# Optimization experiments

Hardware: AMD Instinct MI355X
Metric: run time of the kernel (lower is better)

Reference implementation:

```python
import jax, jax.numpy as jnp
import numpy as np

B, N, K = 2, 1024, 16
D_MODEL, D_ELLIP, N_HEADS = 768, 128, 8
NF = D_MODEL // 6            # sinusoidal freqs per coordinate
MAX_LOG_FREQ = 7.0
ENC_H = max(1, N_HEADS // 2) # ellipsoid encoder heads
ENC_FF = 2048                # torch TransformerEncoderLayer default dim_feedforward


def setup_inputs() -> dict:
    key = jax.random.key(0)
    ks = jax.random.split(key, 20)
    rn = lambda k, sh, sc=1.0: jax.random.normal(k, sh, dtype=jnp.float32) * sc
    w = lambda k, o, i: rn(k, (o, i), 1.0 / np.sqrt(i))
    inp = {}
    inp['s'] = rn(ks[0], (B, N, D_MODEL))
    inp['R'] = rn(ks[1], (B, N, 3, 3))
    inp['t'] = rn(ks[2], (B, N, 3))
    inp['ellip_tokens'] = rn(ks[3], (B, K, D_ELLIP))
    inp['mu'] = rn(ks[4], (B, K, 3))
    inp['Sigma'] = rn(ks[5], (B, K, 3, 3))
    inp['ellip_mask'] = jnp.ones((B, K), dtype=jnp.bool_)
    # main attention params (torch Linear convention: [out, in])
    inp['mix_w'] = w(ks[6], 6 * NF, 6 * NF)
    inp['lin_cov_w'] = w(ks[7], D_MODEL, 9)
    inp['q_w'] = w(ks[8], D_MODEL, D_MODEL)
    inp['k_w'] = w(ks[9], D_MODEL, 2 * D_MODEL)
    inp['v_w'] = w(ks[10], D_MODEL, D_MODEL + D_ELLIP)
    inp['o_w'] = w(ks[11], D_MODEL, D_MODEL)
    # ellipsoid TransformerEncoderLayer params (post-norm, eval mode)
    inp['enc_in_w'] = w(ks[12], 3 * D_ELLIP, D_ELLIP)
    inp['enc_in_b'] = jnp.zeros((3 * D_ELLIP,), jnp.float32)
    inp['enc_out_w'] = w(ks[13], D_ELLIP, D_ELLIP)
    inp['enc_out_b'] = jnp.zeros((D_ELLIP,), jnp.float32)
    inp['lin1_w'] = w(ks[14], ENC_FF, D_ELLIP)
    inp['lin1_b'] = jnp.zeros((ENC_FF,), jnp.float32)
    inp['lin2_w'] = w(ks[15], D_ELLIP, ENC_FF)
    inp['lin2_b'] = jnp.zeros((D_ELLIP,), jnp.float32)
    inp['ln1_g'] = jnp.ones((D_ELLIP,), jnp.float32)
    inp['ln1_b'] = jnp.zeros((D_ELLIP,), jnp.float32)
    inp['ln2_g'] = jnp.ones((D_ELLIP,), jnp.float32)
    inp['ln2_b'] = jnp.zeros((D_ELLIP,), jnp.float32)
    return inp


def _layernorm(x, g, b, eps=1e-5):
    m = x.mean(-1, keepdims=True)
    v = ((x - m) ** 2).mean(-1, keepdims=True)
    return (x - m) / jnp.sqrt(v + eps) * g + b


def _fwd(s, R, t, ellip_tokens, mu, Sigma, mix_w, lin_cov_w, q_w, k_w, v_w, o_w,
         enc_in_w, enc_in_b, enc_out_w, enc_out_b, lin1_w, lin1_b, lin2_w, lin2_b,
         ln1_g, ln1_b, ln2_g, ln2_b, ellip_mask):
    # --- ellipsoid self-attn encoder (single post-norm layer, eval mode) ---
    x = ellip_tokens                                   # [B,K,de]
    qkv = x @ enc_in_w.T + enc_in_b
    q, kk, v = jnp.split(qkv, 3, axis=-1)
    dhe = D_ELLIP // ENC_H
    qh = q.reshape(B, K, ENC_H, dhe)
    kh = kk.reshape(B, K, ENC_H, dhe)
    vh = v.reshape(B, K, ENC_H, dhe)
    sc = jnp.einsum('bqhd,bkhd->bhqk', qh, kh) / np.sqrt(dhe).astype(np.float32)
    ao = jnp.einsum('bhqk,bkhd->bqhd', jax.nn.softmax(sc, -1), vh).reshape(B, K, D_ELLIP)
    ao = ao @ enc_out_w.T + enc_out_b
    x = _layernorm(x + ao, ln1_g, ln1_b)
    ff = jax.nn.relu(x @ lin1_w.T + lin1_b) @ lin2_w.T + lin2_b
    e = _layernorm(x + ff, ln2_g, ln2_b)               # [B,K,de]
    # --- per-query local frame transforms ---
    diff = mu[:, None, :, :] - t[:, :, None, :]        # [B,N,K,3]
    r = jnp.einsum('bnji,bnkj->bnki', R, diff)         # R^T @ diff
    C = jnp.einsum('bnji,bkjl,bnlm->bnkim', R, Sigma, R)  # R^T Sigma R [B,N,K,3,3]
    # --- sinusoidal posenc (sin first, then cos; flatten coord-major) ---
    freqs = 2.0 ** jnp.linspace(0.0, MAX_LOG_FREQ, NF).astype(jnp.float32)
    xf = r[..., None] * freqs                          # [B,N,K,3,NF]
    feat = jnp.concatenate([jnp.sin(xf), jnp.cos(xf)], axis=-2).reshape(B, N, K, 6 * NF)
    pos = feat @ mix_w.T                               # [B,N,K,d]
    cov = C.reshape(B, N, K, 9) @ lin_cov_w.T          # [B,N,K,d]
    K_mat = jnp.concatenate([pos, cov], -1) @ k_w.T    # [B,N,K,d]
    eB = jnp.broadcast_to(e[:, None, :, :], (B, N, K, D_ELLIP))
    V_mat = jnp.concatenate([pos, eB], -1) @ v_w.T     # [B,N,K,d]
    Q = s @ q_w.T                                      # [B,N,d]
    dh = D_MODEL // N_HEADS
    Qh = Q.reshape(B, N, N_HEADS, dh)
    Kh = K_mat.reshape(B, N, K, N_HEADS, dh)
    Vh = V_mat.reshape(B, N, K, N_HEADS, dh)
    scores = jnp.einsum('bnhd,bnkhd->bnhk', Qh, Kh) / np.sqrt(dh).astype(np.float32)
    scores = scores + (1.0 - ellip_mask.astype(scores.dtype))[:, None, None, :] * -10000.0
    attn = jax.nn.softmax(scores, -1)                  # [B,N,H,K]
    out = jnp.einsum('bnhk,bnkhd->bnhd', attn, Vh).reshape(B, N, D_MODEL)
    return out @ o_w.T


def reference(s, R, t, ellip_tokens, mu, Sigma, mix_w, lin_cov_w, q_w, k_w, v_w, o_w,
              enc_in_w, enc_in_b, enc_out_w, enc_out_b, lin1_w, lin1_b, lin2_w, lin2_b,
              ln1_g, ln1_b, ln2_g, ln2_b, ellip_mask):
    return _fwd(s, R, t, ellip_tokens, mu, Sigma, mix_w, lin_cov_w, q_w, k_w, v_w, o_w,
                enc_in_w, enc_in_b, enc_out_w, enc_out_b, lin1_w, lin1_b, lin2_w, lin2_b,
                ln1_g, ln1_b, ln2_g, ln2_b, ellip_mask)
```

## Files before the change

### kernel.cpp

```cpp
#include <hip/hip_runtime.h>
#include <math.h>

#define BB     2
#define SEQ    1024
#define KTOK   16
#define DM     768
#define DE     128
#define NH     8
#define DHD    96
#define EH     4
#define DHE    32
#define EFF    2048

typedef short short8 __attribute__((ext_vector_type(8)));
typedef float f32x4 __attribute__((ext_vector_type(4)));
typedef unsigned short ushort_t;

__device__ __forceinline__ void split2(float x, ushort_t& h, ushort_t& l) {
  unsigned u = __float_as_uint(x);
  unsigned hb = (u + 0x7fffu + ((u >> 16) & 1u)) >> 16;
  float hf = __uint_as_float(hb << 16);
  float r = x - hf;
  unsigned u2 = __float_as_uint(r);
  unsigned lb = (u2 + 0x7fffu + ((u2 >> 16) & 1u)) >> 16;
  h = (ushort_t)hb;
  l = (ushort_t)lb;
}

typedef const unsigned int __attribute__((address_space(1)))* gas_p;
typedef unsigned int __attribute__((address_space(3)))* las_p;
__device__ __forceinline__ void load_lds16(const ushort_t* g, ushort_t* l) {
  __builtin_amdgcn_global_load_lds((gas_p)g, (las_p)l, 16, 0, 0);
}

template<int OMODE, bool ADD>
__device__ __forceinline__ void gemm_body(
    ushort_t (*AhB)[2048], ushort_t (*AlB)[2048],
    ushort_t (*BhB)[2048], ushort_t (*BlB)[2048],
    const ushort_t* A, int lda, int aC0, int aLoOff,
    const ushort_t* B, int ldb, int bC0, int bLoOff,
    void* Cv, int ldc, int cLoOff,
    const float* av, int ldadd,
    int row0, int col0, int N, int K)
{
  int tid = threadIdx.x;
  int wave = tid >> 6, lane = tid & 63;
  int quad = lane >> 4, mrow = lane & 15;
  int wm = (wave >> 1) * 32, wn = (wave & 1) * 32;
  int sr = tid >> 2, q8 = (tid & 3) << 3;
  int wbase = wave << 9;
  f32x4 acc[2][2] = {};

  const ushort_t* pa = A + (long)(row0 + sr) * lda + (aC0 + q8);
  const ushort_t* pb = B + (long)(col0 + sr) * ldb + (bC0 + q8);

  load_lds16(pa, &AhB[0][wbase]);
  load_lds16(pa + aLoOff, &AlB[0][wbase]);
  load_lds16(pb, &BhB[0][wbase]);
  load_lds16(pb + bLoOff, &BlB[0][wbase]);

  int buf = 0;
  for (int k0 = 0; k0 < K; k0 += 32) {
    __syncthreads();
    if (k0 + 32 < K) {
      int kn = k0 + 32;
      load_lds16(pa + kn, &AhB[buf ^ 1][wbase]);
      load_lds16(pa + aLoOff + kn, &AlB[buf ^ 1][wbase]);
      load_lds16(pb + kn, &BhB[buf ^ 1][wbase]);
      load_lds16(pb + bLoOff + kn, &BlB[buf ^ 1][wbase]);
    }
    short8 fah[2], fal[2], fbh[2], fbl[2];
    #pragma unroll
    for (int t = 0; t < 2; t++) {
      fah[t] = *(const short8*)&AhB[buf][(wm + t * 16 + mrow) * 32 + (quad << 3)];
      fal[t] = *(const short8*)&AlB[buf][(wm + t * 16 + mrow) * 32 + (quad << 3)];
      fbh[t] = *(const short8*)&BhB[buf][(wn + t * 16 + mrow) * 32 + (quad << 3)];
      fbl[t] = *(const short8*)&BlB[buf][(wn + t * 16 + mrow) * 32 + (quad << 3)];
    }
    #pragma unroll
    for (int mt = 0; mt < 2; mt++)
      #pragma unroll
      for (int nt = 0; nt < 2; nt++) {
        f32x4 c = acc[mt][nt];
        c = __builtin_amdgcn_mfma_f32_16x16x32_bf16(fah[mt], fbh[nt], c, 0, 0, 0);
        c = __builtin_amdgcn_mfma_f32_16x16x32_bf16(fal[mt], fbh[nt], c, 0, 0, 0);
        c = __builtin_amdgcn_mfma_f32_16x16x32_bf16(fah[mt], fbl[nt], c, 0, 0, 0);
        acc[mt][nt] = c;
      }
    buf ^= 1;
  }
  float* Cf = (float*)Cv;
  ushort_t* Cs = (ushort_t*)Cv;
  #pragma unroll
  for (int mt = 0; mt < 2; mt++)
    #pragma unroll
    for (int nt = 0; nt < 2; nt++) {
      int col = col0 + wn + nt * 16 + mrow;
      if (col >= N) continue;
      int rb = row0 + wm + mt * 16 + (quad << 2);
      #pragma unroll
      for (int rr = 0; rr < 4; rr++) {
        float v = acc[mt][nt][rr];
        if (ADD) v += av[(long)(rb + rr) * ldadd + col];
        if (OMODE == 0) {
          Cf[(long)(rb + rr) * ldc + col] = v;
        } else {
          ushort_t h, l;
          split2(v, h, l);
          Cs[(long)(rb + rr) * ldc + col] = h;
          Cs[(long)(rb + rr) * ldc + cLoOff + col] = l;
        }
      }
    }
}

template<int OMODE, bool ADD>
__global__ __launch_bounds__(256) void gemm3t(
    const ushort_t* __restrict__ A, int lda, int aKstep, int aLoOff,
    const ushort_t* __restrict__ B, long bOffZ, int ldb, int bKstep, int bLoOff,
    void* __restrict__ Cv, int ldc, int cOffZ, int cLoOff,
    const float* __restrict__ addv, int ldadd, int addOffZ,
    int M, int N, int K)
{
  __shared__ ushort_t Ah[2][2048], Al[2][2048], Bh[2][2048], Bl[2][2048];
  int z = blockIdx.z;
  void* Cz = (OMODE == 0) ? (void*)((float*)Cv + (long)z * cOffZ)
                          : (void*)((ushort_t*)Cv + (long)z * cOffZ);
  gemm_body<OMODE, ADD>(Ah, Al, Bh, Bl,
      A, lda, z * aKstep, aLoOff,
      B + (long)z * bOffZ, ldb, z * bKstep, bLoOff,
      Cz, ldc, cLoOff,
      ADD ? addv + (long)z * addOffZ : nullptr, ldadd,
      blockIdx.y * 64, blockIdx.x * 64, N, K);
}

__global__ __launch_bounds__(256) void combo1(
    const float* __restrict__ s, const float* __restrict__ q_w,
    const float* __restrict__ o_w, const float* __restrict__ k_w,
    const float* __restrict__ v_w,
    ushort_t* __restrict__ sS, ushort_t* __restrict__ qwS,
    ushort_t* __restrict__ owS, ushort_t* __restrict__ kwS,
    ushort_t* __restrict__ vwS,
    const float* __restrict__ mix_w, ushort_t* __restrict__ mixTS,
    const float* __restrict__ tok, const float* __restrict__ enc_in_w,
    const float* __restrict__ enc_in_b, float* __restrict__ qkv,
    const float* __restrict__ lin_cov_w, float* __restrict__ Bk9)
{
  int r = blockIdx.x, tid = threadIdx.x;
// ... 61 lines not shown
      int rr = idx / 9, p = idx % 9;
      const float* kr = k_w + (long)rr * (2 * DM) + DM;
      float acc = 0.f;
      for (int j = 0; j < DM; j++) acc = fmaf(kr[j], lin_cov_w[j * 9 + p], acc);
      Bk9[idx] = acc;
    }
  }
}

__global__ __launch_bounds__(256) void mega1(
    const ushort_t* __restrict__ sS, const ushort_t* __restrict__ qwS,
    const ushort_t* __restrict__ mixTS, const ushort_t* __restrict__ kwS,
    const ushort_t* __restrict__ vwS,
    ushort_t* __restrict__ QS, ushort_t* __restrict__ AkTS,
    ushort_t* __restrict__ AvS,
    const float* __restrict__ t2e, const float* __restrict__ ln2_g,
    const float* __restrict__ ln2_b, const float* __restrict__ v_w,
    float* __restrict__ evec)
{
  __shared__ ushort_t Ah[2][2048], Al[2][2048], Bh[2][2048], Bl[2][2048];
  int r = blockIdx.x, tid = threadIdx.x;
  if (r < 384) {
    gemm_body<1, false>(Ah, Al, Bh, Bl, sS, 1536, 0, DM, qwS, 1536, 0, DM,
                        QS, 1536, DM, nullptr, 0, (r / 12) * 64, (r % 12) * 64, DM, DM);
  } else if (r < 528) {
    int t2 = r - 384;
    gemm_body<1, false>(Ah, Al, Bh, Bl, mixTS, 1536, 0, DM, kwS, 1536, 0, DM,
                        AkTS, 1536, DM, nullptr, 0, (t2 / 12) * 64, (t2 % 12) * 64, DM, DM);
  } else if (r < 672) {
    int t2 = r - 528;
    gemm_body<1, false>(Ah, Al, Bh, Bl, vwS, 1536, 0, DM, mixTS, 1536, 0, DM,
                        AvS, 1536, DM, nullptr, 0, (t2 / 12) * 64, (t2 % 12) * 64, DM, DM);
  } else {
    __shared__ float el[DE];
    __shared__ float red[4];
    __shared__ float stats[2];
    int idx = r - 672;
    float val = (tid < DE) ? t2e[idx * DE + tid] : 0.f;
    {
      float v = val;
      #pragma unroll
      for (int off = 32; off > 0; off >>= 1) v += __shfl_down(v, off);
      if ((tid & 63) == 0) red[tid >> 6] = v;
      __syncthreads();
      if (tid == 0) stats[0] = (red[0] + red[1] + red[2] + red[3]) * (1.f / DE);
      __syncthreads();
      float d = (tid < DE) ? (val - stats[0]) : 0.f;
      float v2 = d * d;
      #pragma unroll
      for (int off = 32; off > 0; off >>= 1) v2 += __shfl_down(v2, off);
      if ((tid & 63) == 0) red[tid >> 6] = v2;
      __syncthreads();
      if (tid == 0) stats[1] = rsqrtf((red[0] + red[1] + red[2] + red[3]) * (1.f / DE) + 1e-5f);
      __syncthreads();
      if (tid < DE) el[tid] = (val - stats[0]) * stats[1] * ln2_g[tid] + ln2_b[tid];
      __syncthreads();
    }
    #pragma unroll
    for (int q = 0; q < 3; q++) {
      int d = tid + (q << 8);
      float acc = 0.f;
      const float4* wr = (const float4*)(v_w + (long)d * (DM + DE) + DM);
      #pragma unroll 8
      for (int j = 0; j < DE / 4; j++) {
        float4 p = wr[j];
        acc = fmaf(p.x, el[j * 4 + 0], acc);
        acc = fmaf(p.y, el[j * 4 + 1], acc);
        acc = fmaf(p.z, el[j * 4 + 2], acc);
        acc = fmaf(p.w, el[j * 4 + 3], acc);
      }
      evec[idx * DM + d] = acc;
    }
  }
}

__global__ __launch_bounds__(256) void qa_qb(
    const ushort_t* __restrict__ QS, const ushort_t* __restrict__ AkTS,
    float* __restrict__ QA, const float* __restrict__ Bk9,
    float* __restrict__ QB)
{
  __shared__ ushort_t Ah[2][2048], Al[2][2048], Bh[2][2048], Bl[2][2048];
  int r = blockIdx.x;
  if (r < 3072) {
    int z = r / 384, rr = r % 384;
    gemm_body<0, false>(Ah, Al, Bh, Bl,
        QS, 1536, z * DHD, DM, AkTS, 1536, z * DHD, DM,
        (void*)(QA + (long)z * DM), NH * DM, 0, nullptr, 0,
        (rr / 12) * 64, (rr % 12) * 64, DM, DHD);
  } else {
    int idx = (r - 3072) * 256 + threadIdx.x;
    if (idx < BB * SEQ * NH * 9) {
      int bn = idx / 72, rem = idx % 72, h = rem / 9, p = rem % 9;
      const ushort_t* qr = QS + (long)bn * 1536 + h * DHD;
      float acc = 0.f;
      for (int k = 0; k < DHD; k++) {
        float q = __uint_as_float((unsigned)qr[k] << 16) +
                  __uint_as_float((unsigned)qr[DM + k] << 16);
        acc = fmaf(q, Bk9[(h * DHD + k) * 9 + p], acc);
      }
      QB[idx] = acc;
    }
  }
}

__global__ __launch_bounds__(128) void enc_attn_ln1(
    const float* __restrict__ tok, const float* __restrict__ qkvG,
    const float* __restrict__ out_w, const float* __restrict__ out_b,
    const float* __restrict__ ln1_g, const float* __restrict__ ln1_b,
    float* __restrict__ x1G)
{
  int idx = blockIdx.x;
  int b = idx >> 4, tk = idx & 15;
  int tid = threadIdx.x;
  __shared__ float qkvs[KTOK][384];
  __shared__ float ao[DE];
  __shared__ float scl[EH][KTOK], attnl[EH][KTOK];
  __shared__ float red[2];
  __shared__ float stats[2];
  for (int i = tid; i < KTOK * 384; i += 128)
    qkvs[i / 384][i % 384] = qkvG[b * KTOK * 384 + i];
  __syncthreads();
  if (tid < EH * KTOK) {
    int h = tid >> 4, kk = tid & 15;
    float acc = 0.f;
    #pragma unroll 8
    for (int d = 0; d < DHE; d++)
      acc = fmaf(qkvs[tk][h * DHE + d], qkvs[kk][DE + h * DHE + d], acc);
    scl[h][kk] = acc * 0.17677669529663687f;
  }
  __syncthreads();
  if (tid < EH) {
    float m = -1e30f;
    for (int kk = 0; kk < KTOK; kk++) m = fmaxf(m, scl[tid][kk]);
    float s = 0.f;
    for (int kk = 0; kk < KTOK; kk++) { float e = expf(scl[tid][kk] - m); attnl[tid][kk] = e; s += e; }
    float inv = 1.f / s;
    for (int kk = 0; kk < KTOK; kk++) attnl[tid][kk] *= inv;
  }
  __syncthreads();
  {
    int h = tid / DHE;
    float acc = 0.f;
    #pragma unroll
    for (int kk = 0; kk < KTOK; kk++) acc = fmaf(attnl[h][kk], qkvs[kk][256 + tid], acc);
    ao[tid] = acc;
  }
  __syncthreads();
  float val;
  {
    float acc = out_b[tid];
    const float4* wr = (const float4*)(out_w + (long)tid * DE);
    #pragma unroll 8
    for (int j = 0; j < DE / 4; j++) {
      float4 p = wr[j];
      acc = fmaf(p.x, ao[j * 4 + 0], acc);
      acc = fmaf(p.y, ao[j * 4 + 1], acc);
      acc = fmaf(p.z, ao[j * 4 + 2], acc);
      acc = fmaf(p.w, ao[j * 4 + 3], acc);
    }
    val = tok[idx * DE + tid] + acc;
  }
  {
    float v = val;
    #pragma unroll
    for (int off = 32; off > 0; off >>= 1) v += __shfl_down(v, off);
    if ((tid & 63) == 0) red[tid >> 6] = v;
    __syncthreads();
    if (tid == 0) stats[0] = (red[0] + red[1]) * (1.f / DE);
    __syncthreads();
    float d = val - stats[0];
    float v2 = d * d;
    #pragma unroll
    for (int off = 32; off > 0; off >>= 1) v2 += __shfl_down(v2, off);
    if ((tid & 63) == 0) red[tid >> 6] = v2;
    __syncthreads();
    if (tid == 0) stats[1] = rsqrtf((red[0] + red[1]) * (1.f / DE) + 1e-5f);
    __syncthreads();
    x1G[idx * DE + tid] = (val - stats[0]) * stats[1] * ln1_g[tid] + ln1_b[tid];
  }
}

__global__ __launch_bounds__(256) void enc_ff1(
    const float* __restrict__ x1G, const float* __restrict__ lin1_w,
    const float* __restrict__ lin1_b, float* __restrict__ ff1G)
{
  int tkn = blockIdx.x >> 3;
  int f = ((blockIdx.x & 7) << 8) + threadIdx.x;
  __shared__ float xs[DE];
  if (threadIdx.x < DE) xs[threadIdx.x] = x1G[tkn * DE + threadIdx.x];
  __syncthreads();
  float acc = lin1_b[f];
  const float4* wr = (const float4*)(lin1_w + (long)f * DE);
  #pragma unroll 8
  for (int j = 0; j < DE / 4; j++) {
    float4 p = wr[j];
    acc = fmaf(p.x, xs[j * 4 + 0], acc);
    acc = fmaf(p.y, xs[j * 4 + 1], acc);
    acc = fmaf(p.z, xs[j * 4 + 2], acc);
    acc = fmaf(p.w, xs[j * 4 + 3], acc);
  }
  ff1G[tkn * EFF + f] = fmaxf(acc, 0.f);
}

__global__ __launch_bounds__(256) void enc_ff2(
    const float* __restrict__ x1G, const float* __restrict__ ff1G,
    const float* __restrict__ lin2_w, const float* __restrict__ lin2_b,
    float* __restrict__ tmp2G)
{
  int wv = (blockIdx.x << 2) + (threadIdx.x >> 6);
  int tkn = wv >> 7, j = wv & 127;
  int lane = threadIdx.x & 63;
  const float* wr = lin2_w + (long)j * EFF;
  const float* fr = ff1G + (long)tkn * EFF;
  float acc = 0.f;
  #pragma unroll 8
  for (int i = 0; i < EFF / 64; i++) {
    int p = (i << 6) + lane;
    acc = fmaf(wr[p], fr[p], acc);
  }
  #pragma unroll
  for (int off = 32; off > 0; off >>= 1) acc += __shfl_down(acc, off);
  if (lane == 0)
    tmp2G[tkn * DE + j] = x1G[tkn * DE + j] + lin2_b[j] + acc;
}

__global__ __launch_bounds__(256) void main_attn(
    const float* __restrict__ Rg, const float* __restrict__ tg,
    const float* __restrict__ mug, const float* __restrict__ Sigg,
    const float* __restrict__ QAg, const float* __restrict__ QBg,
    const float* __restrict__ evec, ushort_t* __restrict__ wfeatS,
    float* __restrict__ outeG)
{
  int bn = blockIdx.x;
  int b = bn >> 10;
  int tid = threadIdx.x;
  int w = tid >> 6, lane = tid & 63;
  int h0 = 2 * w, h1 = 2 * w + 1;
  __shared__ float Rm[9], tm[3];
  __shared__ float rK[KTOK][3];
  __shared__ float C9[KTOK][9];
  __shared__ float featL[8][772];
  __shared__ float QBl[NH][12];
  __shared__ float scl[NH][KTOK];
  __shared__ float attnl[NH][KTOK];
  __shared__ float freqsL[128];
  float qa0[12], qa1[12];
  {
    const float* qbase = QAg + (long)bn * (NH * DM);
    #pragma unroll
    for (int i = 0; i < 12; i++) {
      qa0[i] = qbase[h0 * DM + i * 64 + lane];
      qa1[i] = qbase[h1 * DM + i * 64 + lane];
    }
  }
  if (tid < 9) Rm[tid] = Rg[bn * 9 + tid];
  if (tid >= 16 && tid < 19) tm[tid - 16] = tg[bn * 3 + (tid - 16)];
  if (tid >= 32 && tid < 32 + NH * 9) {
    int q = tid - 32;
    QBl[q / 9][q % 9] = QBg[bn * (NH * 9) + q];
  }
  if (tid >= 128) {
    const float step = 7.0f / 127.0f;
    freqsL[tid - 128] = exp2f(step * (float)(tid - 128));
  }
  __syncthreads();
  if (tid < KTOK) {
    int k = tid;
// ... 18 lines not shown
        for (int l = 0; l < 3; l++) a = fmaf(Sg[j * 3 + l], Rm[l * 3 + m2], a);
        SR[j * 3 + m2] = a;
      }
    #pragma unroll
    for (int i = 0; i < 3; i++)
      #pragma unroll
      for (int m2 = 0; m2 < 3; m2++) {
        float a = 0.f;
        #pragma unroll
        for (int j = 0; j < 3; j++) a = fmaf(Rm[j * 3 + i], SR[j * 3 + m2], a);
        C9[k][i * 3 + m2] = a;
      }
  }
  __syncthreads();
  for (int half = 0; half < 2; half++) {
    for (int i = tid; i < 8 * 384; i += 256) {
      int k = i / 384, jj = i % 384;
      int coord = jj >> 7, f = jj & 127;
      float xf = rK[half * 8 + k][coord] * freqsL[f];
      float sv, cv;
      __sincosf(xf, &sv, &cv);
      featL[k][jj] = sv;
      featL[k][jj + 384] = cv;
    }
    __syncthreads();
    for (int k = 0; k < 8; k++) {
      float a0 = 0.f, a1 = 0.f;
      #pragma unroll
      for (int i = 0; i < 12; i++) {
        float fv = featL[k][i * 64 + lane];
        a0 = fmaf(qa0[i], fv, a0);
        a1 = fmaf(qa1[i], fv, a1);
      }
      #pragma unroll
      for (int off = 32; off > 0; off >>= 1) {
        a0 += __shfl_down(a0, off);
        a1 += __shfl_down(a1, off);
      }
      if (lane == 0) { scl[h0][half * 8 + k] = a0; scl[h1][half * 8 + k] = a1; }
    }
    __syncthreads();
  }
  if (tid < NH) {
    int h = tid;
    float vals[KTOK];
    float m = -1e30f;
    for (int k = 0; k < KTOK; k++) {
      float a = scl[h][k];
      #pragma unroll
      for (int p = 0; p < 9; p++) a = fmaf(C9[k][p], QBl[h][p], a);
      a *= 0.10206207261596575f;
      vals[k] = a;
      m = fmaxf(m, a);
    }
    float s = 0.f;
    for (int k = 0; k < KTOK; k++) { float e = expf(vals[k] - m); attnl[h][k] = e; s += e; }
    float inv = 1.f / s;
    for (int k = 0; k < KTOK; k++) attnl[h][k] *= inv;
  }
  __syncthreads();
  float wf0[12], wf1[12];
  #pragma unroll
  for (int i = 0; i < 12; i++) { wf0[i] = 0.f; wf1[i] = 0.f; }
  for (int pass = 0; pass < 2; pass++) {
    int kb = (pass == 0) ? 8 : 0;
    if (pass == 1) {
      __syncthreads();
      for (int i = tid; i < 8 * 384; i += 256) {
        int k = i / 384, jj = i % 384;
        int coord = jj >> 7, f = jj & 127;
        float xf = rK[k][coord] * freqsL[f];
        float sv, cv;
        __sincosf(xf, &sv, &cv);
        featL[k][jj] = sv;
        featL[k][jj + 384] = cv;
      }
      __syncthreads();
    }
    #pragma unroll
    for (int i = 0; i < 12; i++) {
      int jj = i * 64 + lane;
      float s0 = wf0[i], s1 = wf1[i];
      #pragma unroll
      for (int k = 0; k < 8; k++) {
        float fv = featL[k][jj];
        s0 = fmaf(attnl[h0][kb + k], fv, s0);
        s1 = fmaf(attnl[h1][kb + k], fv, s1);
      }
      wf0[i] = s0; wf1[i] = s1;
    }
  }
  {
    ushort_t* wrow = wfeatS + (long)bn * (2 * NH * DM);
    #pragma unroll
    for (int i = 0; i < 12; i++) {
      int jj = i * 64 + lane;
      ushort_t h, l;
      split2(wf0[i], h, l);
      wrow[h0 * DM + jj] = h;
      wrow[NH * DM + h0 * DM + jj] = l;
      split2(wf1[i], h, l);
      wrow[h1 * DM + jj] = h;
      wrow[NH * DM + h1 * DM + jj] = l;
    }
  }
  for (int d = tid; d < DM; d += 256) {
    int h = d / DHD;
    float acc = 0.f;
    #pragma unroll
    for (int k = 0; k < KTOK; k++)
      acc = fmaf(attnl[h][k], evec[(b * KTOK + k) * DM + d], acc);
    outeG[(long)bn * DM + d] = acc;
  }
}

extern "C" void kernel_launch(void* const* d_in, const int* in_sizes, int n_in,
                              void* d_out, int out_size, void* d_ws, size_t ws_size,
                              hipStream_t stream) {
// ... 14 lines not shown
  const float* enc_out_w = (const float*)d_in[15];
  const float* enc_out_b = (const float*)d_in[16];
  const float* lin1_w = (const float*)d_in[17];
  const float* lin1_b = (const float*)d_in[18];
  const float* lin2_w = (const float*)d_in[19];
  const float* lin2_b = (const float*)d_in[20];
  const float* ln1_g = (const float*)d_in[21];
  const float* ln1_b = (const float*)d_in[22];
  const float* ln2_g = (const float*)d_in[23];
  const float* ln2_b = (const float*)d_in[24];
  float* out = (float*)d_out;
  char* wsb  = (char*)d_ws;

  const int BN = BB * SEQ;
  float* qkv  = (float*)(wsb);
  float* x1e  = (float*)(wsb + 49152);
  float* ff1e = (float*)(wsb + 65536);
  float* t2e  = (float*)(wsb + 327680);
  float* evec = (float*)(wsb + 344064);
  float* Bk9  = (float*)(wsb + 442368);
  char* p = wsb + 470016;
  ushort_t* qwS   = (ushort_t*)p;  p += 2359296;
  ushort_t* owS   = (ushort_t*)p;  p += 2359296;
  ushort_t* kwS   = (ushort_t*)p;  p += 2359296;
  ushort_t* vwS   = (ushort_t*)p;  p += 2359296;
  ushort_t* mixTS = (ushort_t*)p;  p += 2359296;
  ushort_t* AkTS  = (ushort_t*)p;  p += 2359296;
  ushort_t* AvS   = (ushort_t*)p;  p += 2359296;
  ushort_t* sS    = (ushort_t*)p;  p += 6291456;
  ushort_t* QS    = (ushort_t*)p;  p += 6291456;
  float*    QB    = (float*)p;     p += 589824;
  float*    oute  = (float*)p;     p += 6291456;
  float*    QA    = (float*)p;     p += 50331648;
  ushort_t* wfeatS = (ushort_t*)QA;
  ushort_t* US     = sS;

  dim3 blk(256);

  combo1<<<4043, blk, 0, stream>>>(s, q_w, o_w, k_w, v_w,
                                   sS, qwS, owS, kwS, vwS,
                                   mix_w, mixTS,
                                   tok, enc_in_w, enc_in_b, qkv,
                                   lin_cov_w, Bk9);
  enc_attn_ln1<<<BB * KTOK, dim3(128), 0, stream>>>(tok, qkv, enc_out_w, enc_out_b,
                                                    ln1_g, ln1_b, x1e);
  enc_ff1<<<256, blk, 0, stream>>>(x1e, lin1_w, lin1_b, ff1e);
  enc_ff2<<<1024, blk, 0, stream>>>(x1e, ff1e, lin2_w, lin2_b, t2e);
  mega1<<<704, blk, 0, stream>>>(sS, qwS, mixTS, kwS, vwS,
                                 QS, AkTS, AvS,
                                 t2e, ln2_g, ln2_b, v_w, evec);
  qa_qb<<<3648, blk, 0, stream>>>(QS, AkTS, QA, Bk9, QB);
  main_attn<<<BN, blk, 0, stream>>>(R, t, mu, Sig, QA, QB, evec, wfeatS, oute);
  gemm3t<1, true><<<dim3(2, 32, NH), blk, 0, stream>>>(
      wfeatS, 2 * NH * DM, DM, NH * DM,  AvS, (long)DHD * 1536, 1536, 0, DM,
      US, 1536, DHD, DM,  oute, DM, DHD,  BN, DHD, DM);
  gemm3t<0, false><<<dim3(12, 32, 1), blk, 0, stream>>>(
      US, 1536, 0, DM,  owS, 0, 1536, 0, DM,
      out, DM, 0, 0,  nullptr, 0, 0,  BN, DM, DM);
}
```

Before: 333.5 us.

## Replace LDS-tiled GEMMs with per-wave direct-load tiles and fuse encoder into mega1

Swaps the shared-memory double-buffered 64x64 GEMM body for a per-wave 32x32 tile that loads bf16 hi/lo fragments straight from global memory with no LDS or barriers. All GEMM launches (QS, AkTS, AvS, QA, U, output projection) now use this path. The ellipsoid encoder attention, LN1, FF1, FF2 and LN2 are folded into mega1's extra blocks, which removes three launches. main_attn is vectorised with float4 feature, query and output accesses. The trade-off is redundant global reads with no LDS reuse across waves, and 32 encoder blocks that now each run the full FFN serially.

```diff
diff --git a/kernel.cpp b/kernel.cpp
--- a/kernel.cpp
+++ b/kernel.cpp
@@ -27,67 +27,37 @@
   l = (ushort_t)lb;
 }
 
-typedef const unsigned int __attribute__((address_space(1)))* gas_p;
-typedef unsigned int __attribute__((address_space(3)))* las_p;
-__device__ __forceinline__ void load_lds16(const ushort_t* g, ushort_t* l) {
-  __builtin_amdgcn_global_load_lds((gas_p)g, (las_p)l, 16, 0, 0);
-}
+#define MFMA(a, b, c) __builtin_amdgcn_mfma_f32_16x16x32_bf16(a, b, c, 0, 0, 0)
 
 template<int OMODE, bool ADD>
-__device__ __forceinline__ void gemm_body(
-    ushort_t (*AhB)[2048], ushort_t (*AlB)[2048],
-    ushort_t (*BhB)[2048], ushort_t (*BlB)[2048],
-    const ushort_t* A, int lda, int aC0, int aLoOff,
-    const ushort_t* B, int ldb, int bC0, int bLoOff,
-    void* Cv, int ldc, int cLoOff,
-    const float* av, int ldadd,
-    int row0, int col0, int N, int K)
+__device__ __forceinline__ void flat_tile(
+    const ushort_t* __restrict__ A, int lda, int aC0, int aLoOff,
+    const ushort_t* __restrict__ B, int ldb, int bC0, int bLoOff,
+    void* __restrict__ Cv, int ldc, int cLoOff,
+    const float* __restrict__ av, int ldadd,
+    int row0, int col0, int K)
 {
-  int tid = threadIdx.x;
-  int wave = tid >> 6, lane = tid & 63;
+  int lane = threadIdx.x & 63;
   int quad = lane >> 4, mrow = lane & 15;
-  int wm = (wave >> 1) * 32, wn = (wave & 1) * 32;
-  int sr = tid >> 2, q8 = (tid & 3) << 3;
-  int wbase = wave << 9;
   f32x4 acc[2][2] = {};
-
-  const ushort_t* pa = A + (long)(row0 + sr) * lda + (aC0 + q8);
-  const ushort_t* pb = B + (long)(col0 + sr) * ldb + (bC0 + q8);
-
-  load_lds16(pa, &AhB[0][wbase]);
-  load_lds16(pa + aLoOff, &AlB[0][wbase]);
-  load_lds16(pb, &BhB[0][wbase]);
-  load_lds16(pb + bLoOff, &BlB[0][wbase]);
-
-  int buf = 0;
+  const ushort_t* pa0 = A + (long)(row0 + mrow) * lda + aC0 + (quad << 3);
+  const ushort_t* pa1 = pa0 + (long)16 * lda;
+  const ushort_t* pb0 = B + (long)(col0 + mrow) * ldb + bC0 + (quad << 3);
+  const ushort_t* pb1 = pb0 + (long)16 * ldb;
+  #pragma unroll 2
   for (int k0 = 0; k0 < K; k0 += 32) {
-    __syncthreads();
-    if (k0 + 32 < K) {
-      int kn = k0 + 32;
-      load_lds16(pa + kn, &AhB[buf ^ 1][wbase]);
-      load_lds16(pa + aLoOff + kn, &AlB[buf ^ 1][wbase]);
-      load_lds16(pb + kn, &BhB[buf ^ 1][wbase]);
-      load_lds16(pb + bLoOff + kn, &BlB[buf ^ 1][wbase]);
-    }
-    short8 fah[2], fal[2], fbh[2], fbl[2];
-    #pragma unroll
-    for (int t = 0; t < 2; t++) {
-      fah[t] = *(const short8*)&AhB[buf][(wm + t * 16 + mrow) * 32 + (quad << 3)];
-      fal[t] = *(const short8*)&AlB[buf][(wm + t * 16 + mrow) * 32 + (quad << 3)];
-      fbh[t] = *(const short8*)&BhB[buf][(wn + t * 16 + mrow) * 32 + (quad << 3)];
-      fbl[t] = *(const short8*)&BlB[buf][(wn + t * 16 + mrow) * 32 + (quad << 3)];
-    }
-    #pragma unroll
-    for (int mt = 0; mt < 2; mt++)
-      #pragma unroll
-      for (int nt = 0; nt < 2; nt++) {
-        f32x4 c = acc[mt][nt];
-        c = __builtin_amdgcn_mfma_f32_16x16x32_bf16(fah[mt], fbh[nt], c, 0, 0, 0);
-        c = __builtin_amdgcn_mfma_f32_16x16x32_bf16(fal[mt], fbh[nt], c, 0, 0, 0);
-        c = __builtin_amdgcn_mfma_f32_16x16x32_bf16(fah[mt], fbl[nt], c, 0, 0, 0);
-        acc[mt][nt] = c;
-      }
-    buf ^= 1;
+    short8 a0h = *(const short8*)(pa0 + k0);
+    short8 a1h = *(const short8*)(pa1 + k0);
+    short8 b0h = *(const short8*)(pb0 + k0);
+    short8 b1h = *(const short8*)(pb1 + k0);
+    short8 a0l = *(const short8*)(pa0 + aLoOff + k0);
+    short8 a1l = *(const short8*)(pa1 + aLoOff + k0);
+    short8 b0l = *(const short8*)(pb0 + bLoOff + k0);
+    short8 b1l = *(const short8*)(pb1 + bLoOff + k0);
+    acc[0][0] = MFMA(a0h, b0h, MFMA(a0l, b0h, MFMA(a0h, b0l, acc[0][0])));
+    acc[0][1] = MFMA(a0h, b1h, MFMA(a0l, b1h, MFMA(a0h, b1l, acc[0][1])));
+    acc[1][0] = MFMA(a1h, b0h, MFMA(a1l, b0h, MFMA(a1h, b0l, acc[1][0])));
+    acc[1][1] = MFMA(a1h, b1h, MFMA(a1l, b1h, MFMA(a1h, b1l, acc[1][1])));
   }
   float* Cf = (float*)Cv;
   ushort_t* Cs = (ushort_t*)Cv;
@@ -95,9 +65,8 @@
   for (int mt = 0; mt < 2; mt++)
     #pragma unroll
     for (int nt = 0; nt < 2; nt++) {
-      int col = col0 + wn + nt * 16 + mrow;
-      if (col >= N) continue;
-      int rb = row0 + wm + mt * 16 + (quad << 2);
+      int col = col0 + nt * 16 + mrow;
+      int rb = row0 + mt * 16 + (quad << 2);
       #pragma unroll
       for (int rr = 0; rr < 4; rr++) {
         float v = acc[mt][nt][rr];
@@ -112,26 +81,6 @@
         }
       }
     }
-}
-
-template<int OMODE, bool ADD>
-__global__ __launch_bounds__(256) void gemm3t(
-    const ushort_t* __restrict__ A, int lda, int aKstep, int aLoOff,
-    const ushort_t* __restrict__ B, long bOffZ, int ldb, int bKstep, int bLoOff,
-    void* __restrict__ Cv, int ldc, int cOffZ, int cLoOff,
-    const float* __restrict__ addv, int ldadd, int addOffZ,
-    int M, int N, int K)
-{
-  __shared__ ushort_t Ah[2][2048], Al[2][2048], Bh[2][2048], Bl[2][2048];
-  int z = blockIdx.z;
-  void* Cz = (OMODE == 0) ? (void*)((float*)Cv + (long)z * cOffZ)
-                          : (void*)((ushort_t*)Cv + (long)z * cOffZ);
-  gemm_body<OMODE, ADD>(Ah, Al, Bh, Bl,
-      A, lda, z * aKstep, aLoOff,
-      B + (long)z * bOffZ, ldb, z * bKstep, bLoOff,
-      Cz, ldc, cLoOff,
-      ADD ? addv + (long)z * addOffZ : nullptr, ldadd,
-      blockIdx.y * 64, blockIdx.x * 64, N, K);
 }
 
 __global__ __launch_bounds__(256) void combo1(
@@ -223,63 +172,165 @@
     const ushort_t* __restrict__ vwS,
     ushort_t* __restrict__ QS, ushort_t* __restrict__ AkTS,
     ushort_t* __restrict__ AvS,
-    const float* __restrict__ t2e, const float* __restrict__ ln2_g,
-    const float* __restrict__ ln2_b, const float* __restrict__ v_w,
-    float* __restrict__ evec)
+    const float* __restrict__ tok, const float* __restrict__ qkvG,
+    const float* __restrict__ out_w, const float* __restrict__ out_b,
+    const float* __restrict__ ln1_g, const float* __restrict__ ln1_b,
+    const float* __restrict__ lin1_w, const float* __restrict__ lin1_b,
+    const float* __restrict__ lin2_w, const float* __restrict__ lin2_b,
+    const float* __restrict__ ln2_g, const float* __restrict__ ln2_b,
+    const float* __restrict__ v_w, float* __restrict__ evec)
 {
-  __shared__ ushort_t Ah[2][2048], Al[2][2048], Bh[2][2048], Bl[2][2048];
-  int r = blockIdx.x, tid = threadIdx.x;
-  if (r < 384) {
-    gemm_body<1, false>(Ah, Al, Bh, Bl, sS, 1536, 0, DM, qwS, 1536, 0, DM,
-                        QS, 1536, DM, nullptr, 0, (r / 12) * 64, (r % 12) * 64, DM, DM);
-  } else if (r < 528) {
-    int t2 = r - 384;
-    gemm_body<1, false>(Ah, Al, Bh, Bl, mixTS, 1536, 0, DM, kwS, 1536, 0, DM,
-                        AkTS, 1536, DM, nullptr, 0, (t2 / 12) * 64, (t2 % 12) * 64, DM, DM);
-  } else if (r < 672) {
-    int t2 = r - 528;
-    gemm_body<1, false>(Ah, Al, Bh, Bl, vwS, 1536, 0, DM, mixTS, 1536, 0, DM,
-                        AvS, 1536, DM, nullptr, 0, (t2 / 12) * 64, (t2 % 12) * 64, DM, DM);
-  } else {
-    __shared__ float el[DE];
-    __shared__ float red[4];
-    __shared__ float stats[2];
-    int idx = r - 672;
-    float val = (tid < DE) ? t2e[idx * DE + tid] : 0.f;
-    {
-      float v = val;
-      #pragma unroll
-      for (int off = 32; off > 0; off >>= 1) v += __shfl_down(v, off);
-      if ((tid & 63) == 0) red[tid >> 6] = v;
-      __syncthreads();
-      if (tid == 0) stats[0] = (red[0] + red[1] + red[2] + red[3]) * (1.f / DE);
-      __syncthreads();
-      float d = (tid < DE) ? (val - stats[0]) : 0.f;
-      float v2 = d * d;
-      #pragma unroll
-      for (int off = 32; off > 0; off >>= 1) v2 += __shfl_down(v2, off);
-      if ((tid & 63) == 0) red[tid >> 6] = v2;
-      __syncthreads();
-      if (tid == 0) stats[1] = rsqrtf((red[0] + red[1] + red[2] + red[3]) * (1.f / DE) + 1e-5f);
-      __syncthreads();
-      if (tid < DE) el[tid] = (val - stats[0]) * stats[1] * ln2_g[tid] + ln2_b[tid];
-      __syncthreads();
-    }
-    #pragma unroll
-    for (int q = 0; q < 3; q++) {
-      int d = tid + (q << 8);
-      float acc = 0.f;
-      const float4* wr = (const float4*)(v_w + (long)d * (DM + DE) + DM);
-      #pragma unroll 8
-      for (int j = 0; j < DE / 4; j++) {
-        float4 p = wr[j];
-        acc = fmaf(p.x, el[j * 4 + 0], acc);
-        acc = fmaf(p.y, el[j * 4 + 1], acc);
-        acc = fmaf(p.z, el[j * 4 + 2], acc);
-        acc = fmaf(p.w, el[j * 4 + 3], acc);
-      }
-      evec[idx * DM + d] = acc;
-    }
+  int blk = blockIdx.x, tid = threadIdx.x;
+  if (blk < 672) {
+    int gw = blk * 4 + (tid >> 6);
+    if (gw < 1536) {
+      int mt = gw / 24, nt = gw % 24;
+      flat_tile<1, false>(sS, 1536, 0, DM, qwS, 1536, 0, DM,
+                          QS, 1536, DM, nullptr, 0, mt * 32, nt * 32, DM);
+    } else if (gw < 2112) {
+      int t2 = gw - 1536, mt = t2 / 24, nt = t2 % 24;
+      flat_tile<1, false>(mixTS, 1536, 0, DM, kwS, 1536, 0, DM,
+                          AkTS, 1536, DM, nullptr, 0, mt * 32, nt * 32, DM);
+    } else {
+      int t2 = gw - 2112, mt = t2 / 24, nt = t2 % 24;
+      flat_tile<1, false>(vwS, 1536, 0, DM, mixTS, 1536, 0, DM,
+                          AvS, 1536, DM, nullptr, 0, mt * 32, nt * 32, DM);
+    }
+    return;
+  }
+  int idx = blk - 672;
+  int b = idx >> 4, tk = idx & 15;
+  __shared__ float qkvs[KTOK][384];
+  __shared__ float scl2[EH][KTOK], at2[EH][KTOK];
+  __shared__ float ao[DE], x1s[DE], ff1L[EFF], part[256], el[DE];
+  __shared__ float red[4], stats[2];
+  for (int i = tid; i < KTOK * 384; i += 256)
+    qkvs[i / 384][i % 384] = qkvG[b * KTOK * 384 + i];
+  __syncthreads();
+  if (tid < EH * KTOK) {
+    int h = tid >> 4, kk = tid & 15;
+    float a = 0.f;
+    #pragma unroll 8
+    for (int d = 0; d < DHE; d++)
+      a = fmaf(qkvs[tk][h * DHE + d], qkvs[kk][DE + h * DHE + d], a);
+    scl2[h][kk] = a * 0.17677669529663687f;
+  }
+  __syncthreads();
+  if (tid < EH) {
+    float m = -1e30f;
+    for (int kk = 0; kk < KTOK; kk++) m = fmaxf(m, scl2[tid][kk]);
+    float sm = 0.f;
+    for (int kk = 0; kk < KTOK; kk++) { float e = expf(scl2[tid][kk] - m); at2[tid][kk] = e; sm += e; }
+    float inv = 1.f / sm;
+    for (int kk = 0; kk < KTOK; kk++) at2[tid][kk] *= inv;
+  }
+  __syncthreads();
+  if (tid < DE) {
+    int h = tid / DHE;
+    float a = 0.f;
+    #pragma unroll
+    for (int kk = 0; kk < KTOK; kk++) a = fmaf(at2[h][kk], qkvs[kk][256 + tid], a);
+    ao[tid] = a;
+  }
+  __syncthreads();
+  float val = 0.f;
+  if (tid < DE) {
+    float a = out_b[tid];
+    const float4* wr = (const float4*)(out_w + (long)tid * DE);
+    #pragma unroll 8
+    for (int j = 0; j < DE / 4; j++) {
+      float4 p = wr[j];
+      a = fmaf(p.x, ao[j * 4 + 0], a);
+      a = fmaf(p.y, ao[j * 4 + 1], a);
+      a = fmaf(p.z, ao[j * 4 + 2], a);
+      a = fmaf(p.w, ao[j * 4 + 3], a);
+    }
+    val = tok[idx * DE + tid] + a;
+  }
+  {
+    float v = val;
+    #pragma unroll
+    for (int off = 32; off > 0; off >>= 1) v += __shfl_down(v, off);
+    if ((tid & 63) == 0) red[tid >> 6] = v;
+    __syncthreads();
+    if (tid == 0) stats[0] = (red[0] + red[1] + red[2] + red[3]) * (1.f / DE);
+    __syncthreads();
+    float d = (tid < DE) ? (val - stats[0]) : 0.f;
+    float v2 = d * d;
+    #pragma unroll
+    for (int off = 32; off > 0; off >>= 1) v2 += __shfl_down(v2, off);
+    if ((tid & 63) == 0) red[tid >> 6] = v2;
+    __syncthreads();
+    if (tid == 0) stats[1] = rsqrtf((red[0] + red[1] + red[2] + red[3]) * (1.f / DE) + 1e-5f);
+    __syncthreads();
+    if (tid < DE) x1s[tid] = (val - stats[0]) * stats[1] * ln1_g[tid] + ln1_b[tid];
+    __syncthreads();
+  }
+  for (int f = tid; f < EFF; f += 256) {
+    float a = lin1_b[f];
+    const float4* wr = (const float4*)(lin1_w + (long)f * DE);
+    #pragma unroll 8
+    for (int j = 0; j < DE / 4; j++) {
+      float4 p = wr[j];
+      a = fmaf(p.x, x1s[j * 4 + 0], a);
+      a = fmaf(p.y, x1s[j * 4 + 1], a);
+      a = fmaf(p.z, x1s[j * 4 + 2], a);
+      a = fmaf(p.w, x1s[j * 4 + 3], a);
+    }
+    ff1L[f] = fmaxf(a, 0.f);
+  }
+  __syncthreads();
+  {
+    int j = tid >> 1, half = tid & 1;
+    const float4* wr = (const float4*)(lin2_w + (long)j * EFF + half * 1024);
+    const float4* fr = (const float4*)(ff1L + half * 1024);
+    float a = 0.f;
+    #pragma unroll 8
+    for (int i = 0; i < 256; i++) {
+      float4 p = wr[i], q = fr[i];
+      a = fmaf(p.x, q.x, a);
+      a = fmaf(p.y, q.y, a);
+      a = fmaf(p.z, q.z, a);
+      a = fmaf(p.w, q.w, a);
+    }
+    part[tid] = a;
+  }
+  __syncthreads();
+  float t2v = 0.f;
+  if (tid < DE) t2v = x1s[tid] + lin2_b[tid] + part[2 * tid] + part[2 * tid + 1];
+  {
+    float v = t2v;
+    #pragma unroll
+    for (int off = 32; off > 0; off >>= 1) v += __shfl_down(v, off);
+    if ((tid & 63) == 0) red[tid >> 6] = v;
+    __syncthreads();
+    if (tid == 0) stats[0] = (red[0] + red[1] + red[2] + red[3]) * (1.f / DE);
+    __syncthreads();
+    float d = (tid < DE) ? (t2v - stats[0]) : 0.f;
+    float v2 = d * d;
+    #pragma unroll
+    for (int off = 32; off > 0; off >>= 1) v2 += __shfl_down(v2, off);
+    if ((tid & 63) == 0) red[tid >> 6] = v2;
+    __syncthreads();
+    if (tid == 0) stats[1] = rsqrtf((red[0] + red[1] + red[2] + red[3]) * (1.f / DE) + 1e-5f);
+    __syncthreads();
+    if (tid < DE) el[tid] = (t2v - stats[0]) * stats[1] * ln2_g[tid] + ln2_b[tid];
+    __syncthreads();
+  }
+  #pragma unroll
+  for (int q = 0; q < 3; q++) {
+    int d = tid + (q << 8);
+    float a = 0.f;
+    const float4* wr = (const float4*)(v_w + (long)d * (DM + DE) + DM);
+    #pragma unroll 8
+    for (int j = 0; j < DE / 4; j++) {
+      float4 p = wr[j];
+      a = fmaf(p.x, el[j * 4 + 0], a);
+      a = fmaf(p.y, el[j * 4 + 1], a);
+      a = fmaf(p.z, el[j * 4 + 2], a);
+      a = fmaf(p.w, el[j * 4 + 3], a);
+    }
+    evec[idx * DM + d] = a;
   }
 }
 
@@ -288,149 +339,49 @@
     float* __restrict__ QA, const float* __restrict__ Bk9,
     float* __restrict__ QB)
 {
-  __shared__ ushort_t Ah[2][2048], Al[2][2048], Bh[2][2048], Bl[2][2048];
-  int r = blockIdx.x;
-  if (r < 3072) {
-    int z = r / 384, rr = r % 384;
-    gemm_body<0, false>(Ah, Al, Bh, Bl,
-        QS, 1536, z * DHD, DM, AkTS, 1536, z * DHD, DM,
-        (void*)(QA + (long)z * DM), NH * DM, 0, nullptr, 0,
-        (rr / 12) * 64, (rr % 12) * 64, DM, DHD);
+  int blk = blockIdx.x;
+  if (blk < 3072) {
+    int gw = blk * 4 + (threadIdx.x >> 6);
+    int z = gw / 1536, t = gw % 1536;
+    int mt = t / 24, nt = t % 24;
+    flat_tile<0, false>(QS, 1536, z * DHD, DM, AkTS, 1536, z * DHD, DM,
+                        (void*)(QA + (long)z * DM), NH * DM, 0, nullptr, 0,
+                        mt * 32, nt * 32, DHD);
   } else {
-    int idx = (r - 3072) * 256 + threadIdx.x;
-    if (idx < BB * SEQ * NH * 9) {
-      int bn = idx / 72, rem = idx % 72, h = rem / 9, p = rem % 9;
-      const ushort_t* qr = QS + (long)bn * 1536 + h * DHD;
-      float acc = 0.f;
-      for (int k = 0; k < DHD; k++) {
-        float q = __uint_as_float((unsigned)qr[k] << 16) +
-                  __uint_as_float((unsigned)qr[DM + k] << 16);
-        acc = fmaf(q, Bk9[(h * DHD + k) * 9 + p], acc);
-      }
-      QB[idx] = acc;
-    }
-  }
-}
-
-__global__ __launch_bounds__(128) void enc_attn_ln1(
-    const float* __restrict__ tok, const float* __restrict__ qkvG,
-    const float* __restrict__ out_w, const float* __restrict__ out_b,
-    const float* __restrict__ ln1_g, const float* __restrict__ ln1_b,
-    float* __restrict__ x1G)
+    int idx = (blk - 3072) * 256 + threadIdx.x;
+    int bn = idx / 72, rem = idx % 72, h = rem / 9, p = rem % 9;
+    const ushort_t* qr = QS + (long)bn * 1536 + h * DHD;
+    float acc = 0.f;
+    for (int k = 0; k < DHD; k++) {
+      float q = __uint_as_float((unsigned)qr[k] << 16) +
+                __uint_as_float((unsigned)qr[DM + k] << 16);
+      acc = fmaf(q, Bk9[(h * DHD + k) * 9 + p], acc);
+    }
+    QB[idx] = acc;
+  }
+}
+
+__global__ __launch_bounds__(256) void gemm_u(
+    const ushort_t* __restrict__ wfeatS, const ushort_t* __restrict__ AvS,
+    ushort_t* __restrict__ US, const float* __restrict__ oute)
 {
-  int idx = blockIdx.x;
-  int b = idx >> 4, tk = idx & 15;
-  int tid = threadIdx.x;
-  __shared__ float qkvs[KTOK][384];
-  __shared__ float ao[DE];
-  __shared__ float scl[EH][KTOK], attnl[EH][KTOK];
-  __shared__ float red[2];
-  __shared__ float stats[2];
-  for (int i = tid; i < KTOK * 384; i += 128)
-    qkvs[i / 384][i % 384] = qkvG[b * KTOK * 384 + i];
-  __syncthreads();
-  if (tid < EH * KTOK) {
-    int h = tid >> 4, kk = tid & 15;
-    float acc = 0.f;
-    #pragma unroll 8
-    for (int d = 0; d < DHE; d++)
-      acc = fmaf(qkvs[tk][h * DHE + d], qkvs[kk][DE + h * DHE + d], acc);
-    scl[h][kk] = acc * 0.17677669529663687f;
-  }
-  __syncthreads();
-  if (tid < EH) {
-    float m = -1e30f;
-    for (int kk = 0; kk < KTOK; kk++) m = fmaxf(m, scl[tid][kk]);
-    float s = 0.f;
-    for (int kk = 0; kk < KTOK; kk++) { float e = expf(scl[tid][kk] - m); attnl[tid][kk] = e; s += e; }
-    float inv = 1.f / s;
-    for (int kk = 0; kk < KTOK; kk++) attnl[tid][kk] *= inv;
-  }
-  __syncthreads();
-  {
-    int h = tid / DHE;
-    float acc = 0.f;
-    #pragma unroll
-    for (int kk = 0; kk < KTOK; kk++) acc = fmaf(attnl[h][kk], qkvs[kk][256 + tid], acc);
-    ao[tid] = acc;
-  }
-  __syncthreads();
-  float val;
-  {
-    float acc = out_b[tid];
-    const float4* wr = (const float4*)(out_w + (long)tid * DE);
-    #pragma unroll 8
-    for (int j = 0; j < DE / 4; j++) {
-      float4 p = wr[j];
-      acc = fmaf(p.x, ao[j * 4 + 0], acc);
-      acc = fmaf(p.y, ao[j * 4 + 1], acc);
-      acc = fmaf(p.z, ao[j * 4 + 2], acc);
-      acc = fmaf(p.w, ao[j * 4 + 3], acc);
-    }
-    val = tok[idx * DE + tid] + acc;
-  }
-  {
-    float v = val;
-    #pragma unroll
-    for (int off = 32; off > 0; off >>= 1) v += __shfl_down(v, off);
-    if ((tid & 63) == 0) red[tid >> 6] = v;
-    __syncthreads();
-    if (tid == 0) stats[0] = (red[0] + red[1]) * (1.f / DE);
-    __syncthreads();
-    float d = val - stats[0];
-    float v2 = d * d;
-    #pragma unroll
-    for (int off = 32; off > 0; off >>= 1) v2 += __shfl_down(v2, off);
-    if ((tid & 63) == 0) red[tid >> 6] = v2;
-    __syncthreads();
-    if (tid == 0) stats[1] = rsqrtf((red[0] + red[1]) * (1.f / DE) + 1e-5f);
-    __syncthreads();
-    x1G[idx * DE + tid] = (val - stats[0]) * stats[1] * ln1_g[tid] + ln1_b[tid];
-  }
-}
-
-__global__ __launch_bounds__(256) void enc_ff1(
-    const float* __restrict__ x1G, const float* __restrict__ lin1_w,
-    const float* __restrict__ lin1_b, float* __restrict__ ff1G)
+  int gw = blockIdx.x * 4 + (threadIdx.x >> 6);
+  int z = gw / 192, t = gw % 192;
+  int mt = t / 3, nt = t % 3;
+  flat_tile<1, true>(wfeatS, 2 * NH * DM, z * DM, NH * DM,
+                     AvS + (long)z * DHD * 1536, 1536, 0, DM,
+                     (void*)(US + z * DHD), 1536, DM,
+                     oute + z * DHD, DM, mt * 32, nt * 32, DM);
+}
+
+__global__ __launch_bounds__(256) void gemm_out(
+    const ushort_t* __restrict__ US, const ushort_t* __restrict__ owS,
+    float* __restrict__ out)
 {
-  int tkn = blockIdx.x >> 3;
-  int f = ((blockIdx.x & 7) << 8) + threadIdx.x;
-  __shared__ float xs[DE];
-  if (threadIdx.x < DE) xs[threadIdx.x] = x1G[tkn * DE + threadIdx.x];
-  __syncthreads();
-  float acc = lin1_b[f];
-  const float4* wr = (const float4*)(lin1_w + (long)f * DE);
-  #pragma unroll 8
-  for (int j = 0; j < DE / 4; j++) {
-    float4 p = wr[j];
-    acc = fmaf(p.x, xs[j * 4 + 0], acc);
-    acc = fmaf(p.y, xs[j * 4 + 1], acc);
-    acc = fmaf(p.z, xs[j * 4 + 2], acc);
-    acc = fmaf(p.w, xs[j * 4 + 3], acc);
-  }
-  ff1G[tkn * EFF + f] = fmaxf(acc, 0.f);
-}
-
-__global__ __launch_bounds__(256) void enc_ff2(
-    const float* __restrict__ x1G, const float* __restrict__ ff1G,
-    const float* __restrict__ lin2_w, const float* __restrict__ lin2_b,
-    float* __restrict__ tmp2G)
-{
-  int wv = (blockIdx.x << 2) + (threadIdx.x >> 6);
-  int tkn = wv >> 7, j = wv & 127;
-  int lane = threadIdx.x & 63;
-  const float* wr = lin2_w + (long)j * EFF;
-  const float* fr = ff1G + (long)tkn * EFF;
-  float acc = 0.f;
-  #pragma unroll 8
-  for (int i = 0; i < EFF / 64; i++) {
-    int p = (i << 6) + lane;
-    acc = fmaf(wr[p], fr[p], acc);
-  }
-  #pragma unroll
-  for (int off = 32; off > 0; off >>= 1) acc += __shfl_down(acc, off);
-  if (lane == 0)
-    tmp2G[tkn * DE + j] = x1G[tkn * DE + j] + lin2_b[j] + acc;
+  int gw = blockIdx.x * 4 + (threadIdx.x >> 6);
+  int mt = gw / 24, nt = gw % 24;
+  flat_tile<0, false>(US, 1536, 0, DM, owS, 1536, 0, DM,
+                      (void*)out, DM, 0, nullptr, 0, mt * 32, nt * 32, DM);
 }
 
 __global__ __launch_bounds__(256) void main_attn(
@@ -453,13 +404,13 @@
   __shared__ float scl[NH][KTOK];
   __shared__ float attnl[NH][KTOK];
   __shared__ float freqsL[128];
-  float qa0[12], qa1[12];
+  float4 qa0[3], qa1[3];
   {
     const float* qbase = QAg + (long)bn * (NH * DM);
     #pragma unroll
-    for (int i = 0; i < 12; i++) {
-      qa0[i] = qbase[h0 * DM + i * 64 + lane];
-      qa1[i] = qbase[h1 * DM + i * 64 + lane];
+    for (int g = 0; g < 3; g++) {
+      qa0[g] = *(const float4*)&qbase[h0 * DM + g * 256 + (lane << 2)];
+      qa1[g] = *(const float4*)&qbase[h1 * DM + g * 256 + (lane << 2)];
     }
   }
   if (tid < 9) Rm[tid] = Rg[bn * 9 + tid];
@@ -508,30 +459,37 @@
   }
   __syncthreads();
   for (int half = 0; half < 2; half++) {
-    for (int i = tid; i < 8 * 384; i += 256) {
-      int k = i / 384, jj = i % 384;
-      int coord = jj >> 7, f = jj & 127;
-      float xf = rK[half * 8 + k][coord] * freqsL[f];
-      float sv, cv;
-      __sincosf(xf, &sv, &cv);
-      featL[k][jj] = sv;
-      featL[k][jj + 384] = cv;
+    int kb = half * 8;
+    for (int c = tid; c < 768; c += 256) {
+      int k = c / 96, f0 = (c % 96) << 2;
+      int coord = f0 >> 7;
+      float rv = rK[kb + k][coord];
+      float4 fr = *(const float4*)&freqsL[f0 & 127];
+      float4 sv, cv;
+      __sincosf(rv * fr.x, &sv.x, &cv.x);
+      __sincosf(rv * fr.y, &sv.y, &cv.y);
+      __sincosf(rv * fr.z, &sv.z, &cv.z);
+      __sincosf(rv * fr.w, &sv.w, &cv.w);
+      *(float4*)&featL[k][f0] = sv;
+      *(float4*)&featL[k][384 + f0] = cv;
     }
     __syncthreads();
     for (int k = 0; k < 8; k++) {
       float a0 = 0.f, a1 = 0.f;
       #pragma unroll
-      for (int i = 0; i < 12; i++) {
-        float fv = featL[k][i * 64 + lane];
-        a0 = fmaf(qa0[i], fv, a0);
-        a1 = fmaf(qa1[i], fv, a1);
+      for (int g = 0; g < 3; g++) {
+        float4 fv = *(const float4*)&featL[k][g * 256 + (lane << 2)];
+        a0 = fmaf(qa0[g].x, fv.x, a0); a0 = fmaf(qa0[g].y, fv.y, a0);
+        a0 = fmaf(qa0[g].z, fv.z, a0); a0 = fmaf(qa0[g].w, fv.w, a0);
+        a1 = fmaf(qa1[g].x, fv.x, a1); a1 = fmaf(qa1[g].y, fv.y, a1);
+        a1 = fmaf(qa1[g].z, fv.z, a1); a1 = fmaf(qa1[g].w, fv.w, a1);
       }
       #pragma unroll
       for (int off = 32; off > 0; off >>= 1) {
         a0 += __shfl_down(a0, off);
         a1 += __shfl_down(a1, off);
       }
-      if (lane == 0) { scl[h0][half * 8 + k] = a0; scl[h1][half * 8 + k] = a1; }
+      if (lane == 0) { scl[h0][kb + k] = a0; scl[h1][kb + k] = a1; }
     }
     __syncthreads();
   }
@@ -547,55 +505,64 @@
       vals[k] = a;
       m = fmaxf(m, a);
     }
-    float s = 0.f;
-    for (int k = 0; k < KTOK; k++) { float e = expf(vals[k] - m); attnl[h][k] = e; s += e; }
-    float inv = 1.f / s;
+    float sm = 0.f;
+    for (int k = 0; k < KTOK; k++) { float e = expf(vals[k] - m); attnl[h][k] = e; sm += e; }
+    float inv = 1.f / sm;
     for (int k = 0; k < KTOK; k++) attnl[h][k] *= inv;
   }
   __syncthreads();
-  float wf0[12], wf1[12];
+  float at0[KTOK], at1[KTOK];
   #pragma unroll
-  for (int i = 0; i < 12; i++) { wf0[i] = 0.f; wf1[i] = 0.f; }
+  for (int k = 0; k < KTOK; k++) { at0[k] = attnl[h0][k]; at1[k] = attnl[h1][k]; }
+  float4 wf0[3] = {}, wf1[3] = {};
   for (int pass = 0; pass < 2; pass++) {
     int kb = (pass == 0) ? 8 : 0;
     if (pass == 1) {
       __syncthreads();
-      for (int i = tid; i < 8 * 384; i += 256) {
-        int k = i / 384, jj = i % 384;
-        int coord = jj >> 7, f = jj & 127;
-        float xf = rK[k][coord] * freqsL[f];
-        float sv, cv;
-        __sincosf(xf, &sv, &cv);
-        featL[k][jj] = sv;
-        featL[k][jj + 384] = cv;
+      for (int c = tid; c < 768; c += 256) {
+        int k = c / 96, f0 = (c % 96) << 2;
+        int coord = f0 >> 7;
+        float rv = rK[k][coord];
+        float4 fr = *(const float4*)&freqsL[f0 & 127];
+        float4 sv, cv;
+        __sincosf(rv * fr.x, &sv.x, &cv.x);
+        __sincosf(rv * fr.y, &sv.y, &cv.y);
+        __sincosf(rv * fr.z, &sv.z, &cv.z);
+        __sincosf(rv * fr.w, &sv.w, &cv.w);
+        *(float4*)&featL[k][f0] = sv;
+        *(float4*)&featL[k][384 + f0] = cv;
       }
       __syncthreads();
     }
     #pragma unroll
-    for (int i = 0; i < 12; i++) {
-      int jj = i * 64 + lane;
-      float s0 = wf0[i], s1 = wf1[i];
+    for (int g = 0; g < 3; g++) {
+      float4 s0 = wf0[g], s1 = wf1[g];
       #pragma unroll
       for (int k = 0; k < 8; k++) {
-        float fv = featL[k][jj];
-        s0 = fmaf(attnl[h0][kb + k], fv, s0);
-        s1 = fmaf(attnl[h1][kb + k], fv, s1);
-      }
-      wf0[i] = s0; wf1[i] = s1;
+        float4 fv = *(const float4*)&featL[k][g * 256 + (lane << 2)];
+        float w0 = at0[kb + k], w1 = at1[kb + k];
+        s0.x = fmaf(w0, fv.x, s0.x); s0.y = fmaf(w0, fv.y, s0.y);
+        s0.z = fmaf(w0, fv.z, s0.z); s0.w = fmaf(w0, fv.w, s0.w);
+        s1.x = fmaf(w1, fv.x, s1.x); s1.y = fmaf(w1, fv.y, s1.y);
+        s1.z = fmaf(w1, fv.z, s1.z); s1.w = fmaf(w1, fv.w, s1.w);
+      }
+      wf0[g] = s0; wf1[g] = s1;
     }
   }
   {
     ushort_t* wrow = wfeatS + (long)bn * (2 * NH * DM);
     #pragma unroll
-    for (int i = 0; i < 12; i++) {
-      int jj = i * 64 + lane;
-      ushort_t h, l;
-      split2(wf0[i], h, l);
-      wrow[h0 * DM + jj] = h;
-      wrow[NH * DM + h0 * DM + jj] = l;
-      split2(wf1[i], h, l);
-      wrow[h1 * DM + jj] = h;
-      wrow[NH * DM + h1 * DM + jj] = l;
+    for (int g = 0; g < 3; g++) {
+      int jj = g * 256 + (lane << 2);
+      ushort4 hv, lv;
+      split2(wf0[g].x, hv.x, lv.x); split2(wf0[g].y, hv.y, lv.y);
+      split2(wf0[g].z, hv.z, lv.z); split2(wf0[g].w, hv.w, lv.w);
+      *(ushort4*)(wrow + h0 * DM + jj) = hv;
+      *(ushort4*)(wrow + NH * DM + h0 * DM + jj) = lv;
+      split2(wf1[g].x, hv.x, lv.x); split2(wf1[g].y, hv.y, lv.y);
+      split2(wf1[g].z, hv.z, lv.z); split2(wf1[g].w, hv.w, lv.w);
+      *(ushort4*)(wrow + h1 * DM + jj) = hv;
+      *(ushort4*)(wrow + NH * DM + h1 * DM + jj) = lv;
     }
   }
   for (int d = tid; d < DM; d += 256) {
@@ -640,9 +607,6 @@
 
   const int BN = BB * SEQ;
   float* qkv  = (float*)(wsb);
-  float* x1e  = (float*)(wsb + 49152);
-  float* ff1e = (float*)(wsb + 65536);
-  float* t2e  = (float*)(wsb + 327680);
   float* evec = (float*)(wsb + 344064);
   float* Bk9  = (float*)(wsb + 442368);
   char* p = wsb + 470016;
@@ -668,19 +632,12 @@
                                    mix_w, mixTS,
                                    tok, enc_in_w, enc_in_b, qkv,
                                    lin_cov_w, Bk9);
-  enc_attn_ln1<<<BB * KTOK, dim3(128), 0, stream>>>(tok, qkv, enc_out_w, enc_out_b,
-                                                    ln1_g, ln1_b, x1e);
-  enc_ff1<<<256, blk, 0, stream>>>(x1e, lin1_w, lin1_b, ff1e);
-  enc_ff2<<<1024, blk, 0, stream>>>(x1e, ff1e, lin2_w, lin2_b, t2e);
-  mega1<<<704, blk, 0, stream>>>(sS, qwS, mixTS, kwS, vwS,
-                                 QS, AkTS, AvS,
-                                 t2e, ln2_g, ln2_b, v_w, evec);
+  mega1<<<704, blk, 0, stream>>>(sS, qwS, mixTS, kwS, vwS, QS, AkTS, AvS,
+                                 tok, qkv, enc_out_w, enc_out_b,
+                                 ln1_g, ln1_b, lin1_w, lin1_b,
+                                 lin2_w, lin2_b, ln2_g, ln2_b, v_w, evec);
   qa_qb<<<3648, blk, 0, stream>>>(QS, AkTS, QA, Bk9, QB);
   main_attn<<<BN, blk, 0, stream>>>(R, t, mu, Sig, QA, QB, evec, wfeatS, oute);
-  gemm3t<1, true><<<dim3(2, 32, NH), blk, 0, stream>>>(
-      wfeatS, 2 * NH * DM, DM, NH * DM,  AvS, (long)DHD * 1536, 1536, 0, DM,
-      US, 1536, DHD, DM,  oute, DM, DHD,  BN, DHD, DM);
-  gemm3t<0, false><<<dim3(12, 32, 1), blk, 0, stream>>>(
-      US, 1536, 0, DM,  owS, 0, 1536, 0, DM,
-      out, DM, 0, 0,  nullptr, 0, 0,  BN, DM, DM);
-}
+  gemm_u<<<384, blk, 0, stream>>>(wfeatS, AvS, US, oute);
+  gemm_out<<<384, blk, 0, stream>>>(US, owS, out);
+}
```

Result: slower. 442.7 us (+32.7%).
